# Optimization experiments

Hardware: AMD Instinct MI355X
Metric: run time of the kernel (lower is better)

## Reference

```python
import jax, jax.numpy as jnp
import numpy as np

B, M = 2, 8192          # clouds per batch, points per cloud (N = B*M)
K_NEAR, K_FAR, K_SMOOTH = 8, 16, 8
T_LOC, T_CON = 0.1, 0.5
EPS = 1e-8


def setup_inputs() -> dict:
    key = jax.random.key(0)
    k1, k2 = jax.random.split(key)
    scores = jax.random.uniform(k1, (B * M,), dtype=jnp.float32)          # in [0,1]
    coords = jax.random.normal(k2, (B * M, 3), dtype=jnp.float32) * 2.0   # point positions
    batch_ids = (jnp.arange(B * M, dtype=jnp.int32) // M).astype(jnp.int32)
    return {"scores": scores, "coords": coords, "batch_ids": batch_ids}


def _knn_global(coords):
    """Per-cloud brute-force kNN (self included as first neighbor, like pointops.knn_query).
    coords: (N,3) -> global indices (N, K_FAR)."""
    c = coords.reshape(B, M, 3)

    def per_cloud(cb):  # cb: (M,3)
        sq = jnp.sum(cb * cb, axis=-1)                      # (M,)
        d2 = sq[:, None] + sq[None, :] - 2.0 * (cb @ cb.T)  # (M,M) squared dists
        _, idx = jax.lax.top_k(-d2, K_FAR)                  # (M,K_FAR) smallest dists
        return idx

    idx = jax.vmap(per_cloud)(c)                            # (B,M,K_FAR) local indices
    idx = idx + (jnp.arange(B, dtype=idx.dtype) * M)[:, None, None]
    return idx.reshape(B * M, K_FAR)


def _loss_terms(scores, coords, idx):
    # --- locality: neighbors (incl. self) should have similar scores ---
    nb = idx[:, :K_NEAR]                                    # (N,k)
    score_diff = jnp.abs(scores[:, None] - scores[nb])      # (N,k)
    dists = jnp.linalg.norm(coords[:, None, :] - coords[nb], axis=2)  # (N,k)
    w = jnp.exp(-dists / T_LOC)
    loss_loc = jnp.sum(w * score_diff ** 2) / jnp.clip(jnp.sum(w), 1e-8)

    # --- contrastive: near similar, far dissimilar ---
    sim_pos = 1.0 - jnp.abs(scores[:, None] - scores[idx[:, :K_NEAR]])
    sim_neg = 1.0 - jnp.abs(scores[:, None] - scores[idx[:, K_NEAR:K_FAR]])
    loss_pos = -jnp.mean(jnp.log(jax.nn.sigmoid(sim_pos / T_CON) + EPS))
    loss_neg = -jnp.mean(jnp.log(1.0 - jax.nn.sigmoid(sim_neg / T_CON) + EPS))
    loss_con = loss_pos + loss_neg

    # --- distribution: sorted scores match uniform linspace per cloud ---
    sb = jnp.sort(scores.reshape(B, M), axis=1)             # (B,M)
    target = jnp.linspace(0.0, 1.0, M, dtype=scores.dtype)  # (M,)
    loss_dist = jnp.mean(jnp.mean((sb - target[None, :]) ** 2, axis=1))

    # --- smoothness: score close to neighbor mean ---
    nmean = jnp.mean(scores[idx[:, :K_SMOOTH]], axis=1)     # (N,)
    loss_smooth = jnp.mean((scores - nmean) ** 2)

    return loss_loc, loss_con, loss_dist, loss_smooth


def reference(scores, coords, batch_ids):
    del batch_ids  # equal-sized clouds; batch structure is (B, M) by construction
    idx = _knn_global(coords)
    l_loc, l_con, l_dist, l_smooth = _loss_terms(scores, coords, idx)
    total = 1.0 * l_loc + 0.5 * l_con + 0.3 * l_dist + 0.2 * l_smooth
    return total
```

## Files before the change

### kernel.cpp

```cpp
#include <hip/hip_runtime.h>
#include <hip/hip_bf16.h>
#include <math.h>

#define BB 2
#define MM 8192
#define NN (BB * MM)
#define CHUNK 512
#define LOSS_BLOCKS 1024

#define PART_OFF 0
#define RANK_OFF 24576
#define IDX_OFF  90112
#define PK_OFF   1138688

__global__ void prep_kernel(const float* __restrict__ coords, float4* __restrict__ pk) {
    int i = blockIdx.x * blockDim.x + threadIdx.x;
    if (i < NN) {
        float x = coords[3 * i], y = coords[3 * i + 1], z = coords[3 * i + 2];
        float sq = fmaf(x, x, fmaf(y, y, z * z));
        pk[i] = make_float4(x, y, z, sq);
    }
}

__global__ __launch_bounds__(1024) void knn_kernel(const float* __restrict__ scores,
                                                   const float4* __restrict__ pk,
                                                   int* __restrict__ out_idx,
                                                   int* __restrict__ out_rank) {
    __shared__ unsigned lds_k[16][16][64];
    __shared__ int lds_r[16][64];

    const int tid  = threadIdx.x;
    const int lane = tid & 63;
    const int wv   = __builtin_amdgcn_readfirstlane(tid >> 6);
    const int qbase = blockIdx.x * 64;
    const int cbase = (qbase >> 13) << 13;
    const int q = qbase + lane;

    const float4 p = pk[q];
    const float  s = scores[q];
    const float4* __restrict__ pkc = pk + cbase;
    const float*  __restrict__ scc = scores + cbase;

    unsigned slot[16];
#pragma unroll
    for (int k = 0; k < 16; ++k) slot[k] = 0xFFFF0000u + (unsigned)k;
    int rank = 0;

    const int j0 = wv * CHUNK;
    for (int jj = 0; jj < CHUNK; jj += 16) {
        unsigned kb[16];
#pragma unroll
        for (int i = 0; i < 16; ++i) {
            const int j = j0 + jj + i;
            const float4 c = pkc[j];
            const float  sc = scc[j];
            float dot = fmaf(p.x, c.x, fmaf(p.y, c.y, p.z * c.z));
            float d2  = fmaf(-2.0f, dot, p.w + c.w);
            rank += (sc < s) ? 1 : 0;
            kb[i] = (__float_as_uint(d2) & 0xFFFFE000u) | (unsigned)j;
        }
#pragma unroll
        for (int p2 = 1; p2 < 16; p2 <<= 1) {
#pragma unroll
            for (int k2 = p2; k2 >= 1; k2 >>= 1) {
#pragma unroll
                for (int j2 = k2 % p2; j2 + k2 < 16; j2 += 2 * k2) {
#pragma unroll
                    for (int i2 = 0; i2 < k2; ++i2) {
                        if (i2 + j2 + k2 < 16) {
                            if (((i2 + j2) / (2 * p2)) == ((i2 + j2 + k2) / (2 * p2))) {
                                unsigned a = kb[i2 + j2], b = kb[i2 + j2 + k2];
                                kb[i2 + j2]      = min(a, b);
                                kb[i2 + j2 + k2] = max(a, b);
                            }
                        }
                    }
                }
            }
        }
        unsigned m[16];
#pragma unroll
        for (int k = 0; k < 16; ++k) m[k] = min(slot[k], kb[15 - k]);
#pragma unroll
        for (int st = 8; st >= 1; st >>= 1) {
#pragma unroll
            for (int i = 0; i < 16; ++i) {
                if ((i & st) == 0) {
                    unsigned lo = min(m[i], m[i + st]);
                    unsigned hi = max(m[i], m[i + st]);
                    m[i] = lo; m[i + st] = hi;
                }
            }
        }
#pragma unroll
        for (int k = 0; k < 16; ++k) slot[k] = m[k];
    }

#pragma unroll
    for (int k = 0; k < 16; ++k) lds_k[wv][k][lane] = slot[k];
    lds_r[wv][lane] = rank;

    for (int half = 8; half >= 1; half >>= 1) {
        __syncthreads();
        if (wv < half) {
            unsigned a[16], m[16];
#pragma unroll
            for (int k = 0; k < 16; ++k) a[k] = lds_k[wv][k][lane];
#pragma unroll
            for (int k = 0; k < 16; ++k) m[k] = min(a[k], lds_k[wv + half][15 - k][lane]);
#pragma unroll
            for (int st = 8; st >= 1; st >>= 1) {
#pragma unroll
                for (int i = 0; i < 16; ++i) {
                    if ((i & st) == 0) {
                        unsigned lo = min(m[i], m[i + st]);
                        unsigned hi = max(m[i], m[i + st]);
                        m[i] = lo; m[i + st] = hi;
                    }
                }
            }
#pragma unroll
            for (int k = 0; k < 16; ++k) lds_k[wv][k][lane] = m[k];
        }
    }
    __syncthreads();

    if (wv == 0) {
        int rsum = 0;
#pragma unroll
        for (int w = 0; w < 16; ++w) rsum += lds_r[w][lane];
        out_rank[qbase + lane] = rsum;
#pragma unroll
        for (int k = 0; k < 16; ++k)
            out_idx[(qbase + lane) * 16 + k] = (int)(lds_k[0][k][lane] & 0x1FFFu) + cbase;
    }
}

__global__ __launch_bounds__(256) void loss_kernel(const float* __restrict__ scores,
                                                   const float* __restrict__ coords,
                                                   const int* __restrict__ knn,
                                                   const int* __restrict__ rank,
                                                   float* __restrict__ partial) {
    __shared__ float red[4][6];
    const int t = blockIdx.x * 256 + threadIdx.x;
    const int q = t >> 4, k = t & 15;
    const int nb = knn[t];
    const float s  = scores[q];
    const float sn = scores[nb];
    const float diff = fabsf(s - sn);
    const float sim = 1.0f - diff;
    const float sg = 1.0f / (1.0f + expf(-2.0f * sim));

    float a_wd = 0.f, a_w = 0.f, a_pos = 0.f, a_neg = 0.f, snk = 0.f;
    if (k < 8) {
        float cx = coords[3 * q],  cy = coords[3 * q + 1],  cz = coords[3 * q + 2];
        float nx = coords[3 * nb], ny = coords[3 * nb + 1], nz = coords[3 * nb + 2];
        float dx = cx - nx, dy = cy - ny, dz = cz - nz;
        float d = sqrtf(dx * dx + dy * dy + dz * dz);
        float w = expf(-10.0f * d);
        a_wd = w * diff * diff;
        a_w  = w;
        a_pos = logf(sg + 1e-8f);
        snk = sn;
    } else {
        a_neg = logf(1.0f - sg + 1e-8f);
    }

    float nsum = snk;
#pragma unroll
    for (int off = 1; off < 16; off <<= 1) nsum += __shfl_xor(nsum, off);

    float a_sm = 0.f, a_di = 0.f;
    if (k == 0) {
        float t1 = s - nsum * 0.125f;
        a_sm = t1 * t1;
        float t2 = s - (float)rank[q] * (1.0f / 8191.0f);
        a_di = t2 * t2;
    }

#pragma unroll
    for (int off = 1; off < 64; off <<= 1) {
        a_wd  += __shfl_xor(a_wd, off);
        a_w   += __shfl_xor(a_w, off);
        a_pos += __shfl_xor(a_pos, off);
        a_neg += __shfl_xor(a_neg, off);
        a_sm  += __shfl_xor(a_sm, off);
        a_di  += __shfl_xor(a_di, off);
    }
    const int wv = threadIdx.x >> 6;
    if ((threadIdx.x & 63) == 0) {
        red[wv][0] = a_wd; red[wv][1] = a_w; red[wv][2] = a_pos;
        red[wv][3] = a_neg; red[wv][4] = a_sm; red[wv][5] = a_di;
    }
    __syncthreads();
    if (threadIdx.x < 6) {
        float v = red[0][threadIdx.x] + red[1][threadIdx.x] +
                  red[2][threadIdx.x] + red[3][threadIdx.x];
        partial[threadIdx.x * LOSS_BLOCKS + blockIdx.x] = v;
    }
}

__global__ __launch_bounds__(1024) void fin_kernel(const float* __restrict__ partial,
                                                   float* __restrict__ out) {
    __shared__ float red[16][6];
    const int tid = threadIdx.x;
    float a[6];
#pragma unroll
    for (int term = 0; term < 6; ++term) a[term] = partial[term * LOSS_BLOCKS + tid];
#pragma unroll
    for (int off = 1; off < 64; off <<= 1) {
#pragma unroll
        for (int term = 0; term < 6; ++term) a[term] += __shfl_xor(a[term], off);
    }
    if ((tid & 63) == 0) {
#pragma unroll
        for (int term = 0; term < 6; ++term) red[tid >> 6][term] = a[term];
    }
    __syncthreads();
    if (tid == 0) {
        float acc[6];
#pragma unroll
        for (int term = 0; term < 6; ++term) {
            float v = 0.f;
#pragma unroll
            for (int w = 0; w < 16; ++w) v += red[w][term];
            acc[term] = v;
        }
        float l_loc = acc[0] / fmaxf(acc[1], 1e-8f);
        float l_pos = -acc[2] / (float)(NN * 8);
        float l_neg = -acc[3] / (float)(NN * 8);
        float l_sm  = acc[4] / (float)NN;
        float l_di  = acc[5] / (float)NN;
        out[0] = l_loc + 0.5f * (l_pos + l_neg) + 0.3f * l_di + 0.2f * l_sm;
    }
}

extern "C" void kernel_launch(void* const* d_in, const int* in_sizes, int n_in,
                              void* d_out, int out_size, void* d_ws, size_t ws_size,
                              hipStream_t stream) {
    const float* scores = (const float*)d_in[0];
    const float* coords = (const float*)d_in[1];
    (void)in_sizes; (void)n_in; (void)out_size; (void)ws_size;

    char* ws = (char*)d_ws;
    float*  part = (float*)(ws + PART_OFF);
    int*    rank = (int*)(ws + RANK_OFF);
    int*    knn  = (int*)(ws + IDX_OFF);
    float4* pk   = (float4*)(ws + PK_OFF);
    float*  out  = (float*)d_out;

    prep_kernel<<<64, 256, 0, stream>>>(coords, pk);
    knn_kernel<<<256, 1024, 0, stream>>>(scores, pk, knn, rank);
    loss_kernel<<<LOSS_BLOCKS, 256, 0, stream>>>(scores, coords, knn, rank, part);
    fin_kernel<<<1, 1024, 0, stream>>>(part, out);
}
```

Measured before the change: 159.3 us.

## Sort points by Morton cell and prune kNN batches with bounding boxes

Points are bucketed into a per-cloud 16^3 Morton-ordered grid through count, scan and scatter kernels. Each group of 16 sorted points gets a bounding box, and the kNN kernel skips whole batches whose box lower bound exceeds the current 16th-best distance of every lane in the wave, instead of scanning all 8192 candidates. The rank computation moves to a separate kernel over the sorted scores, and the loss reads the sorted arrays. This adds several small kernel launches and atomics, and relies on spatial locality so that wave-level pruning removes most batches.

```diff
diff --git a/kernel.cpp b/kernel.cpp
--- a/kernel.cpp
+++ b/kernel.cpp
@@ -5,100 +5,204 @@
 #define BB 2
 #define MM 8192
 #define NN (BB * MM)
-#define CHUNK 512
+#define NBATCH (NN / 16)
+#define NCELL 4096
 #define LOSS_BLOCKS 1024
 
-#define PART_OFF 0
-#define RANK_OFF 24576
-#define IDX_OFF  90112
-#define PK_OFF   1138688
-
-__global__ void prep_kernel(const float* __restrict__ coords, float4* __restrict__ pk) {
-    int i = blockIdx.x * blockDim.x + threadIdx.x;
+#define PART_OFF   0
+#define RANK_OFF   24576
+#define IDX_OFF    90112
+#define PK_OFF     1138688
+#define SS_OFF     1400832
+#define CELLID_OFF 1466368
+#define CNT_OFF    1531904
+#define CUR_OFF    1564672
+#define BBLO_OFF   1597440
+#define BBHI_OFF   1613824
+
+__device__ __forceinline__ unsigned mort3(unsigned x, unsigned y, unsigned z) {
+    unsigned m = 0;
+#pragma unroll
+    for (int i = 0; i < 4; ++i) {
+        m |= ((x >> i) & 1u) << (3 * i);
+        m |= ((y >> i) & 1u) << (3 * i + 1);
+        m |= ((z >> i) & 1u) << (3 * i + 2);
+    }
+    return m;
+}
+
+__global__ void count_kernel(const float* __restrict__ coords, int* __restrict__ cellid,
+                             int* __restrict__ cnt) {
+    int i = blockIdx.x * 256 + threadIdx.x;
     if (i < NN) {
         float x = coords[3 * i], y = coords[3 * i + 1], z = coords[3 * i + 2];
+        int cx = min(15, max(0, (int)floorf(x) + 8));
+        int cy = min(15, max(0, (int)floorf(y) + 8));
+        int cz = min(15, max(0, (int)floorf(z) + 8));
+        int cid = (i >> 13) * NCELL + (int)mort3((unsigned)cx, (unsigned)cy, (unsigned)cz);
+        cellid[i] = cid;
+        atomicAdd(&cnt[cid], 1);
+    }
+}
+
+__global__ __launch_bounds__(1024) void scan_kernel(const int* __restrict__ cnt,
+                                                    int* __restrict__ cursor) {
+    __shared__ int wsum[16];
+    const int tid = threadIdx.x, lane = tid & 63, wv = tid >> 6;
+    int v[8]; int run = 0;
+#pragma unroll
+    for (int i = 0; i < 8; ++i) { int t = cnt[tid * 8 + i]; v[i] = run; run += t; }
+    int inc = run;
+#pragma unroll
+    for (int off = 1; off < 64; off <<= 1) {
+        int y = __shfl_up(inc, off);
+        if (lane >= off) inc += y;
+    }
+    int laneExcl = inc - run;
+    if (lane == 63) wsum[wv] = inc;
+    __syncthreads();
+    int wbase = 0;
+#pragma unroll
+    for (int w = 0; w < 16; ++w) wbase += (w < wv) ? wsum[w] : 0;
+    const int base = wbase + laneExcl;
+#pragma unroll
+    for (int i = 0; i < 8; ++i) cursor[tid * 8 + i] = base + v[i];
+}
+
+__global__ void scatter_kernel(const float* __restrict__ coords, const float* __restrict__ scores,
+                               const int* __restrict__ cellid, int* __restrict__ cursor,
+                               float4* __restrict__ pk_s, float* __restrict__ s_s) {
+    int i = blockIdx.x * 256 + threadIdx.x;
+    if (i < NN) {
+        int pos = atomicAdd(&cursor[cellid[i]], 1);
+        float x = coords[3 * i], y = coords[3 * i + 1], z = coords[3 * i + 2];
         float sq = fmaf(x, x, fmaf(y, y, z * z));
-        pk[i] = make_float4(x, y, z, sq);
-    }
-}
-
-__global__ __launch_bounds__(1024) void knn_kernel(const float* __restrict__ scores,
-                                                   const float4* __restrict__ pk,
-                                                   int* __restrict__ out_idx,
-                                                   int* __restrict__ out_rank) {
-    __shared__ unsigned lds_k[16][16][64];
-    __shared__ int lds_r[16][64];
-
-    const int tid  = threadIdx.x;
-    const int lane = tid & 63;
-    const int wv   = __builtin_amdgcn_readfirstlane(tid >> 6);
-    const int qbase = blockIdx.x * 64;
-    const int cbase = (qbase >> 13) << 13;
-    const int q = qbase + lane;
-
-    const float4 p = pk[q];
-    const float  s = scores[q];
-    const float4* __restrict__ pkc = pk + cbase;
-    const float*  __restrict__ scc = scores + cbase;
-
-    unsigned slot[16];
-#pragma unroll
-    for (int k = 0; k < 16; ++k) slot[k] = 0xFFFF0000u + (unsigned)k;
-    int rank = 0;
-
-    const int j0 = wv * CHUNK;
-    for (int jj = 0; jj < CHUNK; jj += 16) {
-        unsigned kb[16];
-#pragma unroll
-        for (int i = 0; i < 16; ++i) {
-            const int j = j0 + jj + i;
-            const float4 c = pkc[j];
-            const float  sc = scc[j];
-            float dot = fmaf(p.x, c.x, fmaf(p.y, c.y, p.z * c.z));
-            float d2  = fmaf(-2.0f, dot, p.w + c.w);
-            rank += (sc < s) ? 1 : 0;
-            kb[i] = (__float_as_uint(d2) & 0xFFFFE000u) | (unsigned)j;
-        }
-#pragma unroll
-        for (int p2 = 1; p2 < 16; p2 <<= 1) {
-#pragma unroll
-            for (int k2 = p2; k2 >= 1; k2 >>= 1) {
-#pragma unroll
-                for (int j2 = k2 % p2; j2 + k2 < 16; j2 += 2 * k2) {
-#pragma unroll
-                    for (int i2 = 0; i2 < k2; ++i2) {
-                        if (i2 + j2 + k2 < 16) {
-                            if (((i2 + j2) / (2 * p2)) == ((i2 + j2 + k2) / (2 * p2))) {
-                                unsigned a = kb[i2 + j2], b = kb[i2 + j2 + k2];
-                                kb[i2 + j2]      = min(a, b);
-                                kb[i2 + j2 + k2] = max(a, b);
-                            }
+        pk_s[pos] = make_float4(x, y, z, sq);
+        s_s[pos] = scores[i];
+    }
+}
+
+__global__ void bbox_kernel(const float4* __restrict__ pk_s, float4* __restrict__ bb_lo,
+                            float4* __restrict__ bb_hi) {
+    int b = blockIdx.x * 256 + threadIdx.x;
+    if (b < NBATCH) {
+        float4 c = pk_s[b * 16];
+        float lx = c.x, ly = c.y, lz = c.z, hx = c.x, hy = c.y, hz = c.z;
+#pragma unroll
+        for (int i = 1; i < 16; ++i) {
+            c = pk_s[b * 16 + i];
+            lx = fminf(lx, c.x); ly = fminf(ly, c.y); lz = fminf(lz, c.z);
+            hx = fmaxf(hx, c.x); hy = fmaxf(hy, c.y); hz = fmaxf(hz, c.z);
+        }
+        bb_lo[b] = make_float4(lx, ly, lz, 0.f);
+        bb_hi[b] = make_float4(hx, hy, hz, 0.f);
+    }
+}
+
+__device__ __forceinline__ void sort16(unsigned (&a)[16]) {
+#pragma unroll
+    for (int p2 = 1; p2 < 16; p2 <<= 1) {
+#pragma unroll
+        for (int k2 = p2; k2 >= 1; k2 >>= 1) {
+#pragma unroll
+            for (int j2 = k2 % p2; j2 + k2 < 16; j2 += 2 * k2) {
+#pragma unroll
+                for (int i2 = 0; i2 < k2; ++i2) {
+                    if (i2 + j2 + k2 < 16) {
+                        if (((i2 + j2) / (2 * p2)) == ((i2 + j2 + k2) / (2 * p2))) {
+                            unsigned x = a[i2 + j2], y = a[i2 + j2 + k2];
+                            a[i2 + j2]      = min(x, y);
+                            a[i2 + j2 + k2] = max(x, y);
                         }
                     }
                 }
             }
         }
-        unsigned m[16];
-#pragma unroll
-        for (int k = 0; k < 16; ++k) m[k] = min(slot[k], kb[15 - k]);
-#pragma unroll
-        for (int st = 8; st >= 1; st >>= 1) {
-#pragma unroll
-            for (int i = 0; i < 16; ++i) {
-                if ((i & st) == 0) {
-                    unsigned lo = min(m[i], m[i + st]);
-                    unsigned hi = max(m[i], m[i + st]);
-                    m[i] = lo; m[i + st] = hi;
-                }
+    }
+}
+
+__device__ __forceinline__ void truncmerge(unsigned (&slot)[16], const unsigned (&kb)[16]) {
+    unsigned m[16];
+#pragma unroll
+    for (int k = 0; k < 16; ++k) m[k] = min(slot[k], kb[15 - k]);
+#pragma unroll
+    for (int st = 8; st >= 1; st >>= 1) {
+#pragma unroll
+        for (int i = 0; i < 16; ++i) {
+            if ((i & st) == 0) {
+                unsigned lo = min(m[i], m[i + st]);
+                unsigned hi = max(m[i], m[i + st]);
+                m[i] = lo; m[i + st] = hi;
             }
         }
-#pragma unroll
-        for (int k = 0; k < 16; ++k) slot[k] = m[k];
+    }
+#pragma unroll
+    for (int k = 0; k < 16; ++k) slot[k] = m[k];
+}
+
+__global__ __launch_bounds__(1024) void knn_kernel(const float4* __restrict__ pk_s,
+                                                   const float4* __restrict__ bb_lo,
+                                                   const float4* __restrict__ bb_hi,
+                                                   int* __restrict__ out_idx) {
+    __shared__ unsigned lds_k[16][16][64];
+    const int tid = threadIdx.x, lane = tid & 63;
+    const int wv = __builtin_amdgcn_readfirstlane(tid >> 6);
+    const int qbase = blockIdx.x * 64;
+    const int cloudbase = (qbase >> 13) << 13;
+    const int q = qbase + lane;
+    const float4 p = pk_s[q];
+    const int sb0 = (qbase - cloudbase) >> 4;
+    const float4* __restrict__ pc = pk_s + cloudbase;
+    const int bbase = cloudbase >> 4;
+
+    unsigned slot[16];
+#pragma unroll
+    for (int k = 0; k < 16; ++k) slot[k] = 0x7F000000u + (unsigned)k;
+    float t_f = 3.0e38f;
+
+    auto batch = [&](int bi) {
+        unsigned kb[16];
+#pragma unroll
+        for (int i = 0; i < 16; ++i) {
+            const int j = bi * 16 + i;
+            const float4 c = pc[j];
+            float dot = fmaf(p.x, c.x, fmaf(p.y, c.y, p.z * c.z));
+            float d2  = fmaf(-2.0f, dot, p.w + c.w);
+            kb[i] = (__float_as_uint(d2) & 0xFFFFE000u) | (unsigned)j;
+        }
+        sort16(kb);
+        truncmerge(slot, kb);
+        t_f = fminf(t_f, __uint_as_float((slot[15] & 0xFFFFE000u) + 0x2000u));
+    };
+
+    batch(sb0);
+    batch(sb0 + 1);
+
+    for (int k = 0; k < 32; ++k) {
+        const int bi = wv + (k << 4);
+        if (bi == sb0 || bi == sb0 + 1) continue;
+        const float4 lo = bb_lo[bbase + bi];
+        const float4 hi = bb_hi[bbase + bi];
+        float dx = fmaxf(fmaxf(lo.x - p.x, p.x - hi.x), 0.f);
+        float dy = fmaxf(fmaxf(lo.y - p.y, p.y - hi.y), 0.f);
+        float dz = fmaxf(fmaxf(lo.z - p.z, p.z - hi.z), 0.f);
+        float lb = fmaf(dx, dx, fmaf(dy, dy, dz * dz));
+        if (__any(fmaf(lb, 0.999f, -1e-5f) < t_f)) batch(bi);
+    }
+
+    if (wv != 0) {
+        const unsigned jlo = (unsigned)(sb0 << 4), jhi = jlo + 32u;
+#pragma unroll
+        for (int k = 0; k < 16; ++k) {
+            unsigned j = slot[k] & 0x1FFFu;
+            bool dup = (j >= jlo) && (j < jhi) && (slot[k] < 0x7F000000u);
+            slot[k] = dup ? (0x7F100000u + (unsigned)k) : slot[k];
+        }
+        sort16(slot);
     }
 
 #pragma unroll
     for (int k = 0; k < 16; ++k) lds_k[wv][k][lane] = slot[k];
-    lds_r[wv][lane] = rank;
 
     for (int half = 8; half >= 1; half >>= 1) {
         __syncthreads();
@@ -113,9 +217,9 @@
 #pragma unroll
                 for (int i = 0; i < 16; ++i) {
                     if ((i & st) == 0) {
-                        unsigned lo = min(m[i], m[i + st]);
-                        unsigned hi = max(m[i], m[i + st]);
-                        m[i] = lo; m[i + st] = hi;
+                        unsigned lo2 = min(m[i], m[i + st]);
+                        unsigned hi2 = max(m[i], m[i + st]);
+                        m[i] = lo2; m[i + st] = hi2;
                     }
                 }
             }
@@ -126,18 +230,41 @@
     __syncthreads();
 
     if (wv == 0) {
+#pragma unroll
+        for (int k = 0; k < 16; ++k)
+            out_idx[(qbase + lane) * 16 + k] = (int)(lds_k[0][k][lane] & 0x1FFFu) + cloudbase;
+    }
+}
+
+__global__ __launch_bounds__(1024) void rank_kernel(const float* __restrict__ s_s,
+                                                    int* __restrict__ out_rank) {
+    __shared__ int lds_r[16][64];
+    const int tid = threadIdx.x, lane = tid & 63;
+    const int wv = __builtin_amdgcn_readfirstlane(tid >> 6);
+    const int qbase = blockIdx.x * 64;
+    const int cloudbase = (qbase >> 13) << 13;
+    const float s = s_s[qbase + lane];
+    const float* __restrict__ sc = s_s + cloudbase;
+    int rank = 0;
+    const int j0 = wv * 512;
+    for (int jj = 0; jj < 512; jj += 16) {
+#pragma unroll
+        for (int i = 0; i < 16; ++i) {
+            rank += (sc[j0 + jj + i] < s) ? 1 : 0;
+        }
+    }
+    lds_r[wv][lane] = rank;
+    __syncthreads();
+    if (wv == 0) {
         int rsum = 0;
 #pragma unroll
         for (int w = 0; w < 16; ++w) rsum += lds_r[w][lane];
         out_rank[qbase + lane] = rsum;
-#pragma unroll
-        for (int k = 0; k < 16; ++k)
-            out_idx[(qbase + lane) * 16 + k] = (int)(lds_k[0][k][lane] & 0x1FFFu) + cbase;
-    }
-}
-
-__global__ __launch_bounds__(256) void loss_kernel(const float* __restrict__ scores,
-                                                   const float* __restrict__ coords,
+    }
+}
+
+__global__ __launch_bounds__(256) void loss_kernel(const float* __restrict__ s_s,
+                                                   const float4* __restrict__ pk_s,
                                                    const int* __restrict__ knn,
                                                    const int* __restrict__ rank,
                                                    float* __restrict__ partial) {
@@ -145,17 +272,17 @@
     const int t = blockIdx.x * 256 + threadIdx.x;
     const int q = t >> 4, k = t & 15;
     const int nb = knn[t];
-    const float s  = scores[q];
-    const float sn = scores[nb];
+    const float s  = s_s[q];
+    const float sn = s_s[nb];
     const float diff = fabsf(s - sn);
     const float sim = 1.0f - diff;
     const float sg = 1.0f / (1.0f + expf(-2.0f * sim));
 
     float a_wd = 0.f, a_w = 0.f, a_pos = 0.f, a_neg = 0.f, snk = 0.f;
     if (k < 8) {
-        float cx = coords[3 * q],  cy = coords[3 * q + 1],  cz = coords[3 * q + 2];
-        float nx = coords[3 * nb], ny = coords[3 * nb + 1], nz = coords[3 * nb + 2];
-        float dx = cx - nx, dy = cy - ny, dz = cz - nz;
+        float4 pq = pk_s[q];
+        float4 pn = pk_s[nb];
+        float dx = pq.x - pn.x, dy = pq.y - pn.y, dz = pq.z - pn.z;
         float d = sqrtf(dx * dx + dy * dy + dz * dz);
         float w = expf(-10.0f * d);
         a_wd = w * diff * diff;
@@ -243,14 +370,25 @@
     (void)in_sizes; (void)n_in; (void)out_size; (void)ws_size;
 
     char* ws = (char*)d_ws;
-    float*  part = (float*)(ws + PART_OFF);
-    int*    rank = (int*)(ws + RANK_OFF);
-    int*    knn  = (int*)(ws + IDX_OFF);
-    float4* pk   = (float4*)(ws + PK_OFF);
-    float*  out  = (float*)d_out;
-
-    prep_kernel<<<64, 256, 0, stream>>>(coords, pk);
-    knn_kernel<<<256, 1024, 0, stream>>>(scores, pk, knn, rank);
-    loss_kernel<<<LOSS_BLOCKS, 256, 0, stream>>>(scores, coords, knn, rank, part);
+    float*  part  = (float*)(ws + PART_OFF);
+    int*    rank  = (int*)(ws + RANK_OFF);
+    int*    knn   = (int*)(ws + IDX_OFF);
+    float4* pk_s  = (float4*)(ws + PK_OFF);
+    float*  s_s   = (float*)(ws + SS_OFF);
+    int*    cellid= (int*)(ws + CELLID_OFF);
+    int*    cnt   = (int*)(ws + CNT_OFF);
+    int*    cursor= (int*)(ws + CUR_OFF);
+    float4* bb_lo = (float4*)(ws + BBLO_OFF);
+    float4* bb_hi = (float4*)(ws + BBHI_OFF);
+    float*  out   = (float*)d_out;
+
+    hipMemsetAsync(cnt, 0, 2 * NCELL * sizeof(int), stream);
+    count_kernel<<<64, 256, 0, stream>>>(coords, cellid, cnt);
+    scan_kernel<<<1, 1024, 0, stream>>>(cnt, cursor);
+    scatter_kernel<<<64, 256, 0, stream>>>(coords, scores, cellid, cursor, pk_s, s_s);
+    bbox_kernel<<<4, 256, 0, stream>>>(pk_s, bb_lo, bb_hi);
+    knn_kernel<<<256, 1024, 0, stream>>>(pk_s, bb_lo, bb_hi, knn);
+    rank_kernel<<<256, 1024, 0, stream>>>(s_s, rank);
+    loss_kernel<<<LOSS_BLOCKS, 256, 0, stream>>>(s_s, pk_s, knn, rank, part);
     fin_kernel<<<1, 1024, 0, stream>>>(part, out);
 }
```

Result: faster. 154.9 us (-2.7%).
